# Kernel optimization log

Measured on AMD Instinct MI355X. Metric: run time of the kernel, lower is better.

## Reference

```python
import jax, jax.numpy as jnp
import numpy as np

B, L = 1024, 50
H = 512
N_ITEM, N_ENTITY, N_WORD = 50000, 100000, 30000


def setup_inputs() -> dict:
    key = jax.random.key(0)
    ks = jax.random.split(key, 16)
    inp = {
        "item_ids": jax.random.randint(ks[0], (B, L), 0, N_ITEM),
        "item_len": jax.random.randint(ks[1], (B,), 0, 51),
        "entity_ids": jax.random.randint(ks[2], (B, L), 0, N_ENTITY),
        "entity_len": jax.random.randint(ks[3], (B,), 0, 51),
        "word_ids": jax.random.randint(ks[4], (B, L), 0, N_WORD),
        "word_len": jax.random.randint(ks[5], (B,), 0, 51),
        "labels": jax.random.randint(ks[6], (B,), 0, N_ITEM),
        # learned parameters (torch default-ish init scales)
        "item_emb": jax.random.normal(ks[7], (N_ITEM, H), jnp.float32),
        "entity_emb": jax.random.normal(ks[8], (N_ENTITY, H), jnp.float32),
        "word_emb": jax.random.normal(ks[9], (N_WORD, H), jnp.float32),
        "W1": jax.random.normal(ks[10], (H, 4 * H), jnp.float32) / np.sqrt(H),
        "b1": jnp.zeros((4 * H,), jnp.float32),
        "W2": jax.random.normal(ks[11], (4 * H, N_ITEM), jnp.float32) / np.sqrt(4 * H),
        "b2": jnp.zeros((N_ITEM,), jnp.float32),
    }
    return inp


def _masked_mean(table, ids, lens):
    # segment-mean over ragged lists encoded as padded ids + lengths.
    # empty list -> zeros (matches the torch zero-fallback branch).
    mask = (jnp.arange(L)[None, :] < lens[:, None]).astype(table.dtype)  # [B,L]
    emb = table[ids]                                                     # [B,L,H]
    s = jnp.einsum("blh,bl->bh", emb, mask)
    denom = jnp.maximum(lens, 1).astype(table.dtype)[:, None]
    return s / denom


def reference(item_emb, entity_emb, word_emb, W1, b1, W2, b2,
              item_ids, item_len, entity_ids, entity_len,
              word_ids, word_len, labels):
    u = (_masked_mean(item_emb, item_ids, item_len)
         + _masked_mean(entity_emb, entity_ids, entity_len)
         + _masked_mean(word_emb, word_ids, word_len)) / 3.0   # [B,H]
    h = jax.nn.relu(u @ W1 + b1)                                # [B,4H]
    probs = jax.nn.softmax(h @ W2 + b2, axis=-1)                # [B,n_item]
    # faithful to source: CrossEntropyLoss applied on top of softmax outputs
    logp = jax.nn.log_softmax(probs, axis=-1)
    loss = -jnp.mean(jnp.take_along_axis(logp, labels[:, None], axis=-1))
    return probs, labels, loss
```

## Files before the change

kernel.cpp:

```cpp
#include <hip/hip_runtime.h>
#include <cstdint>
#include <cstddef>

typedef __attribute__((ext_vector_type(8))) short bf16x8;
typedef __attribute__((ext_vector_type(4))) float f32x4;

#define B_DIM 1024
#define L_SEQ 50
#define H_DIM 512
#define NITEM 50000
#define PSTRIDE 400

__device__ __forceinline__ unsigned short f2bf(float x) {
  unsigned u = __float_as_uint(x);
  return (unsigned short)((u + 0x7fffu + ((u >> 16) & 1u)) >> 16);
}
__device__ __forceinline__ unsigned pack2(float lo, float hi) {
  return (unsigned)f2bf(lo) | ((unsigned)f2bf(hi) << 16);
}
__device__ __forceinline__ void gld16(const unsigned short* g, unsigned short* l) {
  __builtin_amdgcn_global_load_lds((const __attribute__((address_space(1))) void*)g,
                                   (__attribute__((address_space(3))) void*)l, 16, 0, 0);
}
#define BAR() asm volatile("s_barrier" ::: "memory")

__device__ __forceinline__ void mean_body(int b2, const int* __restrict__ item_ids,
                                          const int* __restrict__ item_len,
                                          const int* __restrict__ ent_ids,
                                          const int* __restrict__ ent_len,
                                          const int* __restrict__ word_ids,
                                          const int* __restrict__ word_len,
                                          const float* __restrict__ item_emb,
                                          const float* __restrict__ ent_emb,
                                          const float* __restrict__ word_emb,
                                          unsigned short* __restrict__ u_bf) {
  const int b = b2 >> 1;
  const int col = ((b2 & 1) << 8) + threadIdx.x;
  float out = 0.f;
  {
    const int len = item_len[b]; float a = 0.f;
#pragma unroll 4
    for (int l = 0; l < len; ++l) a += item_emb[(size_t)item_ids[b * L_SEQ + l] * H_DIM + col];
    out += a / (float)(len > 0 ? len : 1);
  }
  {
    const int len = ent_len[b]; float a = 0.f;
#pragma unroll 4
    for (int l = 0; l < len; ++l) a += ent_emb[(size_t)ent_ids[b * L_SEQ + l] * H_DIM + col];
    out += a / (float)(len > 0 ? len : 1);
  }
  {
    const int len = word_len[b]; float a = 0.f;
#pragma unroll 4
    for (int l = 0; l < len; ++l) a += word_emb[(size_t)word_ids[b * L_SEQ + l] * H_DIM + col];
    out += a / (float)(len > 0 ? len : 1);
  }
  u_bf[b * H_DIM + col] = f2bf(out / 3.f);
}

__global__ void mean_kernel(const int* __restrict__ item_ids, const int* __restrict__ item_len,
                            const int* __restrict__ ent_ids, const int* __restrict__ ent_len,
                            const int* __restrict__ word_ids, const int* __restrict__ word_len,
                            const float* __restrict__ item_emb, const float* __restrict__ ent_emb,
                            const float* __restrict__ word_emb, unsigned short* __restrict__ u_bf) {
  mean_body(blockIdx.x, item_ids, item_len, ent_ids, ent_len, word_ids, word_len, item_emb,
            ent_emb, word_emb, u_bf);
}

__device__ __forceinline__ void transpose_body(const float* __restrict__ W,
                                               unsigned short* __restrict__ Wt, int K, int N,
                                               int k0, int n0, float (*tile)[65]) {
  const int tn = threadIdx.x & 63, tk = threadIdx.x >> 6;
  const int nv = (n0 + tn < N) ? n0 + tn : N - 1;
#pragma unroll
  for (int i = 0; i < 16; ++i)
    tile[tk + 4 * i][tn] = W[(size_t)(k0 + tk + 4 * i) * N + nv];
  __syncthreads();
  const int rn = threadIdx.x >> 2, ck = (threadIdx.x & 3) * 16;
  if (n0 + rn < N) {
    uint4 o[2];
    unsigned* po = (unsigned*)&o[0];
#pragma unroll
    for (int c = 0; c < 8; ++c)
      po[c] = pack2(tile[ck + 2 * c][rn], tile[ck + 2 * c + 1][rn]);
    *(uint4*)&Wt[(size_t)(n0 + rn) * K + k0 + ck] = o[0];
    *(uint4*)&Wt[(size_t)(n0 + rn) * K + k0 + ck + 8] = o[1];
  }
}

__global__ void prep_kernel(const int* __restrict__ item_ids, const int* __restrict__ item_len,
                            const int* __restrict__ ent_ids, const int* __restrict__ ent_len,
                            const int* __restrict__ word_ids, const int* __restrict__ word_len,
                            const float* __restrict__ item_emb, const float* __restrict__ ent_emb,
                            const float* __restrict__ word_emb, unsigned short* __restrict__ u_bf,
                            const float* __restrict__ W1, unsigned short* __restrict__ W1t,
                            const float* __restrict__ W2, unsigned short* __restrict__ W2t) {
  __shared__ float tile[64][65];
  const int b = blockIdx.x;
  if (b < 2048) {
    mean_body(b, item_ids, item_len, ent_ids, ent_len, word_ids, word_len, item_emb, ent_emb,
              word_emb, u_bf);
  } else if (b < 2048 + 25024) {
    const int t = b - 2048;
    transpose_body(W2, W2t, 2048, NITEM, (t & 31) * 64, (t >> 5) * 64, tile);
  } else {
    const int t = b - (2048 + 25024);
    transpose_body(W1, W1t, 512, 2048, (t & 7) * 64, (t >> 3) * 64, tile);
  }
}

template <int K, int N, int EPI>
__global__ __launch_bounds__(512, 1) void gemm256k(const unsigned short* __restrict__ Ag,
                                                   const unsigned short* __restrict__ Btg,
                                                   const float* __restrict__ bias,
                                                   unsigned short* __restrict__ Cbf,
                                                   float* __restrict__ Cf,
                                                   float* __restrict__ pmax,
                                                   float* __restrict__ psum) {
  __shared__ unsigned short lds[8 * 8192];
  unsigned short* Aring = lds;
  unsigned short* Bring = lds + 4 * 8192;

  const int tid = threadIdx.x;
  const int lane = tid & 63;
  const int wid = tid >> 6;

  const int nwg = gridDim.x;
  const int wgid = (blockIdx.x & 7) * (nwg >> 3) + (blockIdx.x >> 3);
  const int m0 = (wgid & 3) * 256;
  const int panel = wgid >> 2;
  const int n0 = panel * 256;

  const int r0 = (wid * 2) * 16 + (lane >> 2);
  const int r1 = r0 + 16;
  const int cg = (lane & 3) ^ ((lane >> 3) & 3);
  const unsigned short* pa0 = Ag + (size_t)(m0 + r0) * K + cg * 8;
  const unsigned short* pa1 = Ag + (size_t)(m0 + r1) * K + cg * 8;
  int rg0 = n0 + r0; rg0 = rg0 < N ? rg0 : N - 1;
  int rg1 = n0 + r1; rg1 = rg1 < N ? rg1 : N - 1;
  const unsigned short* pb0 = Btg + (size_t)rg0 * K + cg * 8;
  const unsigned short* pb1 = Btg + (size_t)rg1 * K + cg * 8;
  const int li0 = wid * 2, li1 = wid * 2 + 1;

  const int wr = wid >> 2, wc = wid & 3;
  const int l15 = lane & 15, kb = lane >> 4;
  f32x4 acc[8][4] = {};

  const int HS = K / 32;
#pragma unroll
  for (int hh = 0; hh < 3; ++hh) {
    const int ko = hh * 32, sl = hh & 3;
    gld16(pa0 + ko, &Aring[sl * 8192 + li0 * 512]);
    gld16(pa1 + ko, &Aring[sl * 8192 + li1 * 512]);
    gld16(pb0 + ko, &Bring[sl * 8192 + li0 * 512]);
    gld16(pb1 + ko, &Bring[sl * 8192 + li1 * 512]);
  }
  asm volatile("s_waitcnt vmcnt(8)" ::: "memory");
  BAR();

#pragma unroll 1
  for (int h = 0; h < HS; ++h) {
    const int slot = h & 3;
    const int nslot = (h + 3) & 3;
    const int kst = (h + 3) * 32;
    const bool st = (h + 3) < HS;
    const unsigned short* As_ = &Aring[slot * 8192];
    const unsigned short* Bs_ = &Bring[slot * 8192];

    bf16x8 afA[4], bfr[4];
#pragma unroll
    for (int i = 0; i < 4; ++i) {
      const int row = wr * 128 + i * 16 + l15;
      afA[i] = *(const bf16x8*)&As_[row * 32 + (kb ^ ((row >> 1) & 3)) * 8];
    }
#pragma unroll
    for (int j = 0; j < 4; ++j) {
      const int col = wc * 64 + j * 16 + l15;
      bfr[j] = *(const bf16x8*)&Bs_[col * 32 + (kb ^ ((col >> 1) & 3)) * 8];
    }
    if (st) {
      gld16(pa0 + kst, &Aring[nslot * 8192 + li0 * 512]);
      gld16(pa1 + kst, &Aring[nslot * 8192 + li1 * 512]);
    }
    BAR();
    __builtin_amdgcn_s_setprio(1);
#pragma unroll
    for (int i = 0; i < 4; ++i)
#pragma unroll
      for (int j = 0; j < 4; ++j)
        acc[i][j] = __builtin_amdgcn_mfma_f32_16x16x32_bf16(afA[i], bfr[j], acc[i][j], 0, 0, 0);
    __builtin_amdgcn_s_setprio(0);
    BAR();

    bf16x8 afB[4];
#pragma unroll
    for (int i = 0; i < 4; ++i) {
      const int row = wr * 128 + (i + 4) * 16 + l15;
      afB[i] = *(const bf16x8*)&As_[row * 32 + (kb ^ ((row >> 1) & 3)) * 8];
    }
    if (st) {
      gld16(pb0 + kst, &Bring[nslot * 8192 + li0 * 512]);
      gld16(pb1 + kst, &Bring[nslot * 8192 + li1 * 512]);
    }
    BAR();
    __builtin_amdgcn_s_setprio(1);
#pragma unroll
    for (int i = 0; i < 4; ++i)
#pragma unroll
      for (int j = 0; j < 4; ++j)
        acc[i + 4][j] =
            __builtin_amdgcn_mfma_f32_16x16x32_bf16(afB[i], bfr[j], acc[i + 4][j], 0, 0, 0);
    __builtin_amdgcn_s_setprio(0);

    if (h + 1 < HS) {
      if (h + 4 <= HS)
        asm volatile("s_waitcnt vmcnt(8)" ::: "memory");
      else if (h + 3 == HS)
        asm volatile("s_waitcnt vmcnt(4)" ::: "memory");
      else
        asm volatile("s_waitcnt vmcnt(0)" ::: "memory");
      BAR();
    }
  }

  float bv[4];
  bool val[4];
#pragma unroll
  for (int j = 0; j < 4; ++j) {
    const int cgl = n0 + wc * 64 + 16 * j + l15;
    val[j] = (cgl < N);
    bv[j] = bias[val[j] ? cgl : 0];
  }
#pragma unroll
  for (int i = 0; i < 8; ++i) {
    const int rbase = m0 + wr * 128 + 16 * i + 4 * kb;
#pragma unroll
    for (int j = 0; j < 4; ++j) {
      if (val[j]) {
        const int cgl = n0 + wc * 64 + 16 * j + l15;
#pragma unroll
        for (int rr = 0; rr < 4; ++rr) {
          const float v = acc[i][j][rr] + bv[j];
          if (EPI == 0)
            Cbf[(size_t)(rbase + rr) * N + cgl] = f2bf(v > 0.f ? v : 0.f);
          else
            Cf[(size_t)(rbase + rr) * N + cgl] = v;
        }
      }
    }
  }

  if constexpr (EPI == 1) {
    __syncthreads();
    float* redm = (float*)&lds[0];
    float* reds = redm + 1024;
#pragma unroll
    for (int i = 0; i < 8; ++i) {
#pragma unroll
      for (int rr = 0; rr < 4; ++rr) {
        float mx = -3.0e38f;
#pragma unroll
        for (int j = 0; j < 4; ++j)
          if (val[j]) mx = fmaxf(mx, acc[i][j][rr] + bv[j]);
#pragma unroll
        for (int d = 1; d < 16; d <<= 1) mx = fmaxf(mx, __shfl_xor(mx, d));
        float s = 0.f;
#pragma unroll
        for (int j = 0; j < 4; ++j)
          if (val[j]) s += expf(acc[i][j][rr] + bv[j] - mx);
#pragma unroll
        for (int d = 1; d < 16; d <<= 1) s += __shfl_xor(s, d);
        if (l15 == 0) {
          const int rw = wr * 128 + 16 * i + 4 * kb + rr;
          redm[wc * 256 + rw] = mx;
          reds[wc * 256 + rw] = s;
        }
      }
    }
    __syncthreads();
    if (tid < 256) {
      float mm = redm[tid], ss = reds[tid];
#pragma unroll
      for (int w = 1; w < 4; ++w) {
        const float ma = redm[w * 256 + tid], sa = reds[w * 256 + tid];
        const float nm = fmaxf(mm, ma);
        ss = ss * expf(mm - nm) + sa * expf(ma - nm);
        mm = nm;
      }
      pmax[(size_t)(m0 + tid) * PSTRIDE + panel] = mm;
      psum[(size_t)(m0 + tid) * PSTRIDE + panel] = ss;
    }
  }
}

template <int K, int N, int EPI, int PBASE>
__global__ __launch_bounds__(512, 1) void gemm128x256(const unsigned short* __restrict__ Ag,
                                                      const unsigned short* __restrict__ Btg,
                                                      const float* __restrict__ bias,
                                                      unsigned short* __restrict__ Cbf,
                                                      float* __restrict__ Cf,
                                                      float* __restrict__ pmax,
                                                      float* __restrict__ psum) {
  __shared__ unsigned short lds[4 * 4096 + 4 * 8192];
  unsigned short* Aring = lds;
  unsigned short* Bring = lds + 4 * 4096;

  const int tid = threadIdx.x;
  const int lane = tid & 63;
  const int wid = tid >> 6;

  const int nwg = gridDim.x;
  const int wgid = (blockIdx.x & 7) * (nwg >> 3) + (blockIdx.x >> 3);
  const int m0 = (wgid & 7) * 128;
  const int panel = wgid >> 3;
  const int n0 = (PBASE + panel) * 256;

  const int cg = (lane & 3) ^ ((lane >> 3) & 3);
  const int arow = wid * 16 + (lane >> 2);
  const unsigned short* pa = Ag + (size_t)(m0 + arow) * K + cg * 8;
  const int br0 = wid * 32 + (lane >> 2), br1 = br0 + 16;
  int rg0 = n0 + br0; rg0 = rg0 < N ? rg0 : N - 1;
  int rg1 = n0 + br1; rg1 = rg1 < N ? rg1 : N - 1;
  const unsigned short* pb0 = Btg + (size_t)rg0 * K + cg * 8;
  const unsigned short* pb1 = Btg + (size_t)rg1 * K + cg * 8;
  const int li0 = wid * 2, li1 = wid * 2 + 1;

  const int wr = wid >> 2, wc = wid & 3;
  const int l15 = lane & 15, kb = lane >> 4;
  f32x4 acc[4][4] = {};

  const int HS = K / 32;
#pragma unroll
  for (int hh = 0; hh < 3; ++hh) {
    const int ko = hh * 32;
    gld16(pa + ko, &Aring[hh * 4096 + wid * 512]);
    gld16(pb0 + ko, &Bring[hh * 8192 + li0 * 512]);
    gld16(pb1 + ko, &Bring[hh * 8192 + li1 * 512]);
  }
  asm volatile("s_waitcnt vmcnt(6)" ::: "memory");
  BAR();

#pragma unroll 1
  for (int h = 0; h < HS; ++h) {
    const int slot = h & 3;
    const int nslot = (h + 3) & 3;
    const int kst = (h + 3) * 32;
    const unsigned short* As_ = &Aring[slot * 4096];
    const unsigned short* Bs_ = &Bring[slot * 8192];

    if (h + 3 < HS) {
      gld16(pa + kst, &Aring[nslot * 4096 + wid * 512]);
      gld16(pb0 + kst, &Bring[nslot * 8192 + li0 * 512]);
      gld16(pb1 + kst, &Bring[nslot * 8192 + li1 * 512]);
    }

    bf16x8 af[4], bf[4];
#pragma unroll
    for (int i = 0; i < 4; ++i) {
      const int row = wr * 64 + i * 16 + l15;
      af[i] = *(const bf16x8*)&As_[row * 32 + (kb ^ ((row >> 1) & 3)) * 8];
    }
#pragma unroll
    for (int j = 0; j < 4; ++j) {
      const int col = wc * 64 + j * 16 + l15;
      bf[j] = *(const bf16x8*)&Bs_[col * 32 + (kb ^ ((col >> 1) & 3)) * 8];
    }
    __builtin_amdgcn_s_setprio(1);
#pragma unroll
    for (int i = 0; i < 4; ++i)
#pragma unroll
      for (int j = 0; j < 4; ++j)
        acc[i][j] = __builtin_amdgcn_mfma_f32_16x16x32_bf16(af[i], bf[j], acc[i][j], 0, 0, 0);
    __builtin_amdgcn_s_setprio(0);

    if (h + 1 < HS) {
      if (h + 4 <= HS)
        asm volatile("s_waitcnt vmcnt(6)" ::: "memory");
      else if (h + 3 == HS)
        asm volatile("s_waitcnt vmcnt(3)" ::: "memory");
      else
        asm volatile("s_waitcnt vmcnt(0)" ::: "memory");
      BAR();
    }
  }

  float bv[4];
  bool val[4];
#pragma unroll
  for (int j = 0; j < 4; ++j) {
    const int cgl = n0 + wc * 64 + 16 * j + l15;
    val[j] = (cgl < N);
    bv[j] = bias[val[j] ? cgl : 0];
  }
#pragma unroll
  for (int i = 0; i < 4; ++i) {
    const int rbase = m0 + wr * 64 + 16 * i + 4 * kb;
#pragma unroll
    for (int j = 0; j < 4; ++j) {
      if (val[j]) {
        const int cgl = n0 + wc * 64 + 16 * j + l15;
#pragma unroll
        for (int rr = 0; rr < 4; ++rr) {
          const float v = acc[i][j][rr] + bv[j];
          if (EPI == 0)
            Cbf[(size_t)(rbase + rr) * N + cgl] = f2bf(v > 0.f ? v : 0.f);
          else
            Cf[(size_t)(rbase + rr) * N + cgl] = v;
        }
      }
    }
  }

  if constexpr (EPI == 1) {
    __syncthreads();
    float* redm = (float*)&lds[0];
    float* reds = redm + 512;
#pragma unroll
    for (int i = 0; i < 4; ++i) {
#pragma unroll
      for (int rr = 0; rr < 4; ++rr) {
        float mx = -3.0e38f;
#pragma unroll
        for (int j = 0; j < 4; ++j)
          if (val[j]) mx = fmaxf(mx, acc[i][j][rr] + bv[j]);
#pragma unroll
        for (int d = 1; d < 16; d <<= 1) mx = fmaxf(mx, __shfl_xor(mx, d));
        float s = 0.f;
#pragma unroll
        for (int j = 0; j < 4; ++j)
          if (val[j]) s += expf(acc[i][j][rr] + bv[j] - mx);
#pragma unroll
        for (int d = 1; d < 16; d <<= 1) s += __shfl_xor(s, d);
        if (l15 == 0) {
          const int rw = wr * 64 + 16 * i + 4 * kb + rr;
          redm[wc * 128 + rw] = mx;
          reds[wc * 128 + rw] = s;
        }
      }
    }
    __syncthreads();
    if (tid < 128) {
      float mm = redm[tid], ss = reds[tid];
#pragma unroll
      for (int w = 1; w < 4; ++w) {
        const float ma = redm[w * 128 + tid], sa = reds[w * 128 + tid];
        const float nm = fmaxf(mm, ma);
        ss = ss * expf(mm - nm) + sa * expf(ma - nm);
        mm = nm;
      }
      pmax[(size_t)(m0 + tid) * PSTRIDE + PBASE + panel] = mm;
      psum[(size_t)(m0 + tid) * PSTRIDE + PBASE + panel] = ss;
    }
  }
}

template <int K, int N, int EPI>
__global__ __launch_bounds__(256, 2) void gemm128(const unsigned short* __restrict__ Ag,
                                                  const unsigned short* __restrict__ Btg,
                                                  const float* __restrict__ bias,
                                                  unsigned short* __restrict__ Cbf,
                                                  float* __restrict__ Cf) {
  __shared__ unsigned short As[2][128 * 64];
  __shared__ unsigned short Bs[2][128 * 64];
  const int tid = threadIdx.x;
  const int lane = tid & 63;
  const int wid = tid >> 6;
  const int nwg = gridDim.x;
  const int wgid = (blockIdx.x & 7) * (nwg >> 3) + (blockIdx.x >> 3);
  const int m0 = (wgid & 7) * 128;
  const int n0 = (wgid >> 3) * 128;
  const int srsub = lane >> 3;
  const int scg = (lane & 7) ^ srsub;
  const unsigned short* pa[4];
  const unsigned short* pb[4];
#pragma unroll
  for (int qq = 0; qq < 4; ++qq) {
    const int seg = wid * 4 + qq;
    const int row = seg * 8 + srsub;
    pa[qq] = Ag + (size_t)(m0 + row) * K + scg * 8;
    int rg = n0 + row;
    rg = rg < N ? rg : N - 1;
    pb[qq] = Btg + (size_t)rg * K + scg * 8;
  }
  auto stage = [&](int t, int s) {
    const int ko = t * 64;
#pragma unroll
    for (int qq = 0; qq < 4; ++qq) {
      const int seg = wid * 4 + qq;
      gld16(pa[qq] + ko, &As[s][seg * 512]);
      gld16(pb[qq] + ko, &Bs[s][seg * 512]);
    }
  };
  const int wr = wid >> 1, wc = wid & 1;
  const int l15 = lane & 15, kb = lane >> 4;
  f32x4 acc[4][4] = {};
  auto compute = [&](int s) {
#pragma unroll
    for (int koi = 0; koi < 2; ++koi) {
      bf16x8 af[4], bf[4];
#pragma unroll
      for (int i = 0; i < 4; ++i) {
        const int row = wr * 64 + i * 16 + l15;
        af[i] = *(const bf16x8*)&As[s][row * 64 + ((koi * 4 + kb) ^ (row & 7)) * 8];
      }
#pragma unroll
      for (int j = 0; j < 4; ++j) {
        const int col = wc * 64 + j * 16 + l15;
        bf[j] = *(const bf16x8*)&Bs[s][col * 64 + ((koi * 4 + kb) ^ (col & 7)) * 8];
      }
#pragma unroll
      for (int i = 0; i < 4; ++i)
#pragma unroll
        for (int j = 0; j < 4; ++j)
          acc[i][j] = __builtin_amdgcn_mfma_f32_16x16x32_bf16(af[i], bf[j], acc[i][j], 0, 0, 0);
    }
  };
  const int NT = K / 64;
  stage(0, 0);
  asm volatile("s_waitcnt vmcnt(0)" ::: "memory");
  __syncthreads();
#pragma unroll 1
  for (int t = 0; t < NT; ++t) {
    if (t + 1 < NT) stage(t + 1, (t + 1) & 1);
    compute(t & 1);
    asm volatile("s_waitcnt vmcnt(0)" ::: "memory");
    __syncthreads();
  }
  float bv[4];
  bool val[4];
#pragma unroll
  for (int j = 0; j < 4; ++j) {
    const int cg2 = n0 + wc * 64 + 16 * j + l15;
    val[j] = (cg2 < N);
    bv[j] = bias[val[j] ? cg2 : 0];
  }
#pragma unroll
  for (int i = 0; i < 4; ++i) {
    const int rbase = m0 + wr * 64 + 16 * i + 4 * kb;
#pragma unroll
    for (int j = 0; j < 4; ++j) {
      if (val[j]) {
        const int cg2 = n0 + wc * 64 + 16 * j + l15;
#pragma unroll
        for (int rr = 0; rr < 4; ++rr) {
          const float v = acc[i][j][rr] + bv[j];
          if (EPI == 0)
            Cbf[(size_t)(rbase + rr) * N + cg2] = f2bf(v > 0.f ? v : 0.f);
          else
            Cf[(size_t)(rbase + rr) * N + cg2] = v;
        }
      }
    }
  }
}

template <int K, int N, int EPI>
__global__ __launch_bounds__(512, 2) void gemm_fused(const unsigned short* __restrict__ Ag,
                                                     const float* __restrict__ Bg,
                                                     const float* __restrict__ bias,
                                                     unsigned short* __restrict__ Cbf,
                                                     float* __restrict__ Cf,
                                                     float* __restrict__ pmax,
                                                     float* __restrict__ psum) {
  __shared__ unsigned short As[2][256 * 64];
  __shared__ uint4 Bs[2][8 * 128];
  const int tid = threadIdx.x;
  const int lane = tid & 63;
  const int wid = tid >> 6;
  const int m0 = blockIdx.x * 256;
  const int n0 = blockIdx.y * 128;
  const int arow = tid >> 3;
  const int ach = tid & 7;
  const int bn = 2 * lane;
  const int bk = 8 * wid;
  const int bcolg = (n0 + bn < N - 2) ? (n0 + bn) : (N - 2);
  uint4 areg[4];
  float2 breg[8];
  f32x4 acc[4][4] = {};
  auto stage_global = [&](int kt) {
    const int k0 = kt * 64;
#pragma unroll
    for (int qq = 0; qq < 4; ++qq)
      areg[qq] = *(const uint4*)&Ag[(size_t)(m0 + arow + 64 * qq) * K + k0 + 8 * ach];
#pragma unroll
    for (int i = 0; i < 8; ++i) breg[i] = *(const float2*)&Bg[(size_t)(k0 + bk + i) * N + bcolg];
  };
  auto stage_lds = [&](int buf) {
#pragma unroll
    for (int qq = 0; qq < 4; ++qq) {
      const int row = arow + 64 * qq;
      *(uint4*)&As[buf][row * 64 + ((8 * ach) ^ ((row & 7) * 8))] = areg[qq];
    }
    uint4 c0, c1;
    c0.x = pack2(breg[0].x, breg[1].x); c0.y = pack2(breg[2].x, breg[3].x);
    c0.z = pack2(breg[4].x, breg[5].x); c0.w = pack2(breg[6].x, breg[7].x);
    c1.x = pack2(breg[0].y, breg[1].y); c1.y = pack2(breg[2].y, breg[3].y);
    c1.z = pack2(breg[4].y, breg[5].y); c1.w = pack2(breg[6].y, breg[7].y);
    Bs[buf][wid * 128 + bn] = c0;
    Bs[buf][wid * 128 + bn + 1] = c1;
  };
  const int wr = wid & 3, wc = wid >> 2;
  const int mw = 64 * wr, nw = 64 * wc;
  const int l15 = lane & 15, kb = lane >> 4;
  auto compute = [&](int buf) {
#pragma unroll
    for (int koi = 0; koi < 2; ++koi) {
      bf16x8 af[4], bfv[4];
#pragma unroll
      for (int i = 0; i < 4; ++i) {
        const int row = mw + 16 * i + l15;
        af[i] = *(const bf16x8*)&As[buf][row * 64 + ((32 * koi + 8 * kb) ^ ((row & 7) * 8))];
      }
#pragma unroll
      for (int j = 0; j < 4; ++j)
        bfv[j] = *(const bf16x8*)&Bs[buf][(4 * koi + kb) * 128 + nw + 16 * j + l15];
#pragma unroll
      for (int i = 0; i < 4; ++i)
#pragma unroll
        for (int j = 0; j < 4; ++j)
          acc[i][j] = __builtin_amdgcn_mfma_f32_16x16x32_bf16(af[i], bfv[j], acc[i][j], 0, 0, 0);
    }
  };
  const int NT = K / 64;
  stage_global(0);
  stage_lds(0);
  __syncthreads();
  for (int t = 0; t < NT; ++t) {
    const int cur = t & 1;
    if (t + 1 < NT) stage_global(t + 1);
    compute(cur);
    if (t + 1 < NT) stage_lds(cur ^ 1);
    __syncthreads();
  }
  float bv[4];
  bool val[4];
#pragma unroll
  for (int j = 0; j < 4; ++j) {
    const int cg2 = n0 + nw + 16 * j + l15;
    val[j] = (cg2 < N);
    bv[j] = bias[val[j] ? cg2 : 0];
  }
#pragma unroll
  for (int i = 0; i < 4; ++i) {
    const int rbase = m0 + mw + 16 * i + 4 * kb;
#pragma unroll
    for (int j = 0; j < 4; ++j) {
      if (val[j]) {
        const int cg2 = n0 + nw + 16 * j + l15;
#pragma unroll
        for (int rr = 0; rr < 4; ++rr) {
          const float v = acc[i][j][rr] + bv[j];
          if (EPI == 0)
            Cbf[(size_t)(rbase + rr) * N + cg2] = f2bf(v > 0.f ? v : 0.f);
          else
            Cf[(size_t)(rbase + rr) * N + cg2] = v;
        }
      }
    }
  }
  if constexpr (EPI == 1) {
    float* redm = (float*)&As[0][0];
    float* reds = redm + 512;
#pragma unroll
    for (int i = 0; i < 4; ++i) {
#pragma unroll
      for (int rr = 0; rr < 4; ++rr) {
        float mx = -3.0e38f;
#pragma unroll
        for (int j = 0; j < 4; ++j)
          if (val[j]) mx = fmaxf(mx, acc[i][j][rr] + bv[j]);
#pragma unroll
        for (int d = 1; d < 16; d <<= 1) mx = fmaxf(mx, __shfl_xor(mx, d));
        float s = 0.f;
#pragma unroll
        for (int j = 0; j < 4; ++j)
          if (val[j]) s += expf(acc[i][j][rr] + bv[j] - mx);
#pragma unroll
        for (int d = 1; d < 16; d <<= 1) s += __shfl_xor(s, d);
        if (l15 == 0) {
          const int rl = mw + 16 * i + 4 * kb + rr;
          redm[wc * 256 + rl] = mx;
          reds[wc * 256 + rl] = s;
        }
      }
    }
    __syncthreads();
    if (tid < 256) {
      const float ma = redm[tid], mb = redm[256 + tid];
      const float mm = fmaxf(ma, mb);
      const float ss = reds[tid] * expf(ma - mm) + reds[256 + tid] * expf(mb - mm);
      pmax[(size_t)(m0 + tid) * PSTRIDE + blockIdx.y] = mm;
      psum[(size_t)(m0 + tid) * PSTRIDE + blockIdx.y] = ss;
    }
  }
}

__global__ void smax1r(const float* __restrict__ pmax, const float* __restrict__ psum,
                       float* __restrict__ rms, int ntiles) {
  const int b = blockIdx.x;
  const int l = threadIdx.x;
  float m = -3.4e38f, s = 0.f;
  for (int i = l; i < ntiles; i += 64) {
    const float pm = pmax[(size_t)b * PSTRIDE + i];
    const float ps = psum[(size_t)b * PSTRIDE + i];
    const float nm = fmaxf(m, pm);
    s = s * expf(m - nm) + ps * expf(pm - nm);
    m = nm;
  }
  for (int d = 1; d < 64; d <<= 1) {
    const float om = __shfl_xor(m, d), os = __shfl_xor(s, d);
    const float nm = fmaxf(m, om);
    s = s * expf(m - nm) + os * expf(om - nm);
    m = nm;
  }
  if (l == 0) {
    rms[b] = m;
    rms[B_DIM + b] = s;
  }
}

__global__ void smax2(float* __restrict__ buf, const float* __restrict__ rms,
                      const int* __restrict__ labels, float* __restrict__ row_lp) {
  const int b = blockIdx.x;
  float4* p = (float4*)(buf + (size_t)b * NITEM);
  const float m = rms[b];
  const float inv = 1.f / rms[B_DIM + b];
  const int lab = labels[b];
  __shared__ float s_pl;
  __shared__ float ss[256];
  float s2 = 0.f;
  for (int i = threadIdx.x; i < NITEM / 4; i += 256) {
    const float4 v = p[i];
    float pr[4];
#pragma unroll
    for (int j = 0; j < 4; ++j) {
      pr[j] = expf((&v.x)[j] - m) * inv;
      s2 += expf(pr[j] - inv);
    }
    float4 w;
    w.x = pr[0]; w.y = pr[1]; w.z = pr[2]; w.w = pr[3];
    p[i] = w;
    if ((lab >> 2) == i) s_pl = pr[lab & 3];
  }
  ss[threadIdx.x] = s2;
  __syncthreads();
  for (int off = 128; off > 0; off >>= 1) {
    if (threadIdx.x < off) ss[threadIdx.x] += ss[threadIdx.x + off];
    __syncthreads();
  }
  if (threadIdx.x == 0) row_lp[b] = s_pl - (inv + logf(ss[0]));
}

__global__ void fin(const float* __restrict__ row_lp, const int* __restrict__ labels,
                    float* __restrict__ out) {
  __shared__ float sb[256];
  float a = 0.f;
  for (int i = threadIdx.x; i < B_DIM; i += 256) {
    a += row_lp[i];
    out[(size_t)B_DIM * NITEM + i] = (float)labels[i];
  }
  sb[threadIdx.x] = a;
  __syncthreads();
  for (int off = 128; off > 0; off >>= 1) {
    if (threadIdx.x < off) sb[threadIdx.x] += sb[threadIdx.x + off];
    __syncthreads();
  }
  if (threadIdx.x == 0) out[(size_t)B_DIM * NITEM + B_DIM] = -sb[0] / (float)B_DIM;
}

extern "C" void kernel_launch(void* const* d_in, const int* in_sizes, int n_in,
                              void* d_out, int out_size, void* d_ws, size_t ws_size,
                              hipStream_t stream) {
  const int* item_ids = (const int*)d_in[0];
  const int* item_len = (const int*)d_in[1];
  const int* ent_ids = (const int*)d_in[2];
  const int* ent_len = (const int*)d_in[3];
  const int* word_ids = (const int*)d_in[4];
  const int* word_len = (const int*)d_in[5];
  const int* labels = (const int*)d_in[6];
  const float* item_emb = (const float*)d_in[7];
  const float* ent_emb = (const float*)d_in[8];
  const float* word_emb = (const float*)d_in[9];
  const float* W1 = (const float*)d_in[10];
  const float* b1 = (const float*)d_in[11];
  const float* W2 = (const float*)d_in[12];
  const float* b2 = (const float*)d_in[13];

  float* out = (float*)d_out;
  char* ws = (char*)d_ws;
  unsigned short* u_bf = (unsigned short*)ws;
  unsigned short* h_bf = (unsigned short*)(ws + (1 << 20));
  float* pmax = (float*)(ws + 5 * (1 << 20));
  float* psum = (float*)(ws + 7 * (1 << 20));
  float* rms = (float*)(ws + 9 * (1 << 20));
  float* row_lp = rms + 2 * B_DIM;
  unsigned short* W1t = (unsigned short*)(ws + 10 * (1 << 20));
  unsigned short* W2t = (unsigned short*)(ws + 16 * (1 << 20));
  float* logits = out;

  const size_t need = (size_t)16 * (1 << 20) + (size_t)NITEM * 2048 * 2;
  const bool fast = ws_size >= need;

  if (fast) {
    prep_kernel<<<2048 + 25024 + 256, 256, 0, stream>>>(item_ids, item_len, ent_ids, ent_len,
                                                        word_ids, word_len, item_emb, ent_emb,
                                                        word_emb, u_bf, W1, W1t, W2, W2t);
    gemm128<512, 2048, 0><<<8 * 16, 256, 0, stream>>>(u_bf, W1t, b1, h_bf, nullptr);
    gemm256k<2048, NITEM, 1><<<768, 512, 0, stream>>>(h_bf, W2t, b2, nullptr, logits, pmax,
                                                      psum);
    gemm128x256<2048, NITEM, 1, 192><<<32, 512, 0, stream>>>(h_bf, W2t, b2, nullptr, logits,
                                                             pmax, psum);
    smax1r<<<B_DIM, 64, 0, stream>>>(pmax, psum, rms, 196);
  } else {
    mean_kernel<<<2 * B_DIM, 256, 0, stream>>>(item_ids, item_len, ent_ids, ent_len, word_ids,
                                               word_len, item_emb, ent_emb, word_emb, u_bf);
    gemm_fused<512, 2048, 0><<<dim3(4, 16), 512, 0, stream>>>(u_bf, W1, b1, h_bf, nullptr,
                                                              nullptr, nullptr);
    gemm_fused<2048, NITEM, 1><<<dim3(4, 391), 512, 0, stream>>>(h_bf, W2, b2, nullptr, logits,
                                                                 pmax, psum);
    smax1r<<<B_DIM, 64, 0, stream>>>(pmax, psum, rms, 391);
  }
  smax2<<<B_DIM, 256, 0, stream>>>(logits, rms, labels, row_lp);
  fin<<<1, 256, 0, stream>>>(row_lp, labels, out);
}
```

Baseline: 562.3 us.

## Load B operand directly from global into registers, staging only A in LDS

The big W2 GEMM now streams B fragments from global memory straight into registers, double-buffered across even and odd k-steps, and stages only the A tile in an LDS ring. This halves LDS usage and drops the mid-step barriers and B LDS reads, leaving one barrier per k-step. The cost is that every wave of the four in a column re-reads the same B columns from global or L2 without LDS sharing, and the B loads are uncoalesced 16-byte per-lane accesses with the latency held in registers.

```diff
diff --git a/kernel.cpp b/kernel.cpp
--- a/kernel.cpp
+++ b/kernel.cpp
@@ -110,16 +110,14 @@
 }
 
 template <int K, int N, int EPI>
-__global__ __launch_bounds__(512, 1) void gemm256k(const unsigned short* __restrict__ Ag,
+__global__ __launch_bounds__(512, 1) void gemm256r(const unsigned short* __restrict__ Ag,
                                                    const unsigned short* __restrict__ Btg,
                                                    const float* __restrict__ bias,
                                                    unsigned short* __restrict__ Cbf,
                                                    float* __restrict__ Cf,
                                                    float* __restrict__ pmax,
                                                    float* __restrict__ psum) {
-  __shared__ unsigned short lds[8 * 8192];
-  unsigned short* Aring = lds;
-  unsigned short* Bring = lds + 4 * 8192;
+  __shared__ unsigned short Aring[4 * 8192];
 
   const int tid = threadIdx.x;
   const int lane = tid & 63;
@@ -131,97 +129,87 @@
   const int panel = wgid >> 2;
   const int n0 = panel * 256;
 
-  const int r0 = (wid * 2) * 16 + (lane >> 2);
+  const int r0 = wid * 32 + (lane >> 2);
   const int r1 = r0 + 16;
   const int cg = (lane & 3) ^ ((lane >> 3) & 3);
   const unsigned short* pa0 = Ag + (size_t)(m0 + r0) * K + cg * 8;
   const unsigned short* pa1 = Ag + (size_t)(m0 + r1) * K + cg * 8;
-  int rg0 = n0 + r0; rg0 = rg0 < N ? rg0 : N - 1;
-  int rg1 = n0 + r1; rg1 = rg1 < N ? rg1 : N - 1;
-  const unsigned short* pb0 = Btg + (size_t)rg0 * K + cg * 8;
-  const unsigned short* pb1 = Btg + (size_t)rg1 * K + cg * 8;
   const int li0 = wid * 2, li1 = wid * 2 + 1;
 
   const int wr = wid >> 2, wc = wid & 3;
   const int l15 = lane & 15, kb = lane >> 4;
+
+  const unsigned short* pbf[4];
+#pragma unroll
+  for (int j = 0; j < 4; ++j) {
+    int r = n0 + wc * 64 + 16 * j + l15;
+    r = r < N ? r : N - 1;
+    pbf[j] = Btg + (size_t)r * K + kb * 8;
+  }
+
   f32x4 acc[8][4] = {};
+  uint4 bE[4], bO[4];
 
   const int HS = K / 32;
 #pragma unroll
-  for (int hh = 0; hh < 3; ++hh) {
-    const int ko = hh * 32, sl = hh & 3;
-    gld16(pa0 + ko, &Aring[sl * 8192 + li0 * 512]);
-    gld16(pa1 + ko, &Aring[sl * 8192 + li1 * 512]);
-    gld16(pb0 + ko, &Bring[sl * 8192 + li0 * 512]);
-    gld16(pb1 + ko, &Bring[sl * 8192 + li1 * 512]);
-  }
-  asm volatile("s_waitcnt vmcnt(8)" ::: "memory");
+  for (int j = 0; j < 4; ++j) bE[j] = *(const uint4*)&pbf[j][0];
+#pragma unroll
+  for (int j = 0; j < 4; ++j) bO[j] = *(const uint4*)&pbf[j][32];
+  gld16(pa0, &Aring[li0 * 512]);
+  gld16(pa1, &Aring[li1 * 512]);
+  gld16(pa0 + 32, &Aring[8192 + li0 * 512]);
+  gld16(pa1 + 32, &Aring[8192 + li1 * 512]);
+  gld16(pa0 + 64, &Aring[2 * 8192 + li0 * 512]);
+  gld16(pa1 + 64, &Aring[2 * 8192 + li1 * 512]);
+  asm volatile("s_waitcnt vmcnt(0)" ::: "memory");
   BAR();
 
+#define GSTEP(h, bcur)                                                                   \
+  {                                                                                      \
+    const unsigned short* As_ = &Aring[((h) & 3) * 8192];                                \
+    bf16x8 af[8];                                                                        \
+    _Pragma("unroll") for (int i = 0; i < 8; ++i) {                                      \
+      const int row = wr * 128 + i * 16 + l15;                                           \
+      af[i] = *(const bf16x8*)&As_[row * 32 + (kb ^ ((row >> 1) & 3)) * 8];              \
+    }                                                                                    \
+    __builtin_amdgcn_s_setprio(1);                                                       \
+    _Pragma("unroll") for (int i = 0; i < 8; ++i) {                                      \
+      acc[i][0] = __builtin_amdgcn_mfma_f32_16x16x32_bf16(af[i], *(bf16x8*)&bcur[0],     \
+                                                          acc[i][0], 0, 0, 0);           \
+      acc[i][1] = __builtin_amdgcn_mfma_f32_16x16x32_bf16(af[i], *(bf16x8*)&bcur[1],     \
+                                                          acc[i][1], 0, 0, 0);           \
+      acc[i][2] = __builtin_amdgcn_mfma_f32_16x16x32_bf16(af[i], *(bf16x8*)&bcur[2],     \
+                                                          acc[i][2], 0, 0, 0);           \
+      acc[i][3] = __builtin_amdgcn_mfma_f32_16x16x32_bf16(af[i], *(bf16x8*)&bcur[3],     \
+                                                          acc[i][3], 0, 0, 0);           \
+    }                                                                                    \
+    __builtin_amdgcn_s_setprio(0);                                                       \
+    if ((h) + 2 < HS) {                                                                  \
+      _Pragma("unroll") for (int j = 0; j < 4; ++j) bcur[j] =                            \
+          *(const uint4*)&pbf[j][((h) + 2) * 32];                                        \
+    }                                                                                    \
+    if ((h) + 3 < HS) {                                                                  \
+      unsigned short* d = &Aring[(((h) + 3) & 3) * 8192];                                \
+      gld16(pa0 + ((h) + 3) * 32, d + li0 * 512);                                        \
+      gld16(pa1 + ((h) + 3) * 32, d + li1 * 512);                                        \
+    }                                                                                    \
+    if ((h) + 1 < HS) {                                                                  \
+      if ((h) + 4 <= HS)                                                                 \
+        asm volatile("s_waitcnt vmcnt(6)" ::: "memory");                                 \
+      else if ((h) + 3 == HS)                                                            \
+        asm volatile("s_waitcnt vmcnt(4)" ::: "memory");                                 \
+      else                                                                               \
+        asm volatile("s_waitcnt vmcnt(0)" ::: "memory");                                 \
+      BAR();                                                                             \
+    }                                                                                    \
+  }
+
 #pragma unroll 1
-  for (int h = 0; h < HS; ++h) {
-    const int slot = h & 3;
-    const int nslot = (h + 3) & 3;
-    const int kst = (h + 3) * 32;
-    const bool st = (h + 3) < HS;
-    const unsigned short* As_ = &Aring[slot * 8192];
-    const unsigned short* Bs_ = &Bring[slot * 8192];
-
-    bf16x8 afA[4], bfr[4];
-#pragma unroll
-    for (int i = 0; i < 4; ++i) {
-      const int row = wr * 128 + i * 16 + l15;
-      afA[i] = *(const bf16x8*)&As_[row * 32 + (kb ^ ((row >> 1) & 3)) * 8];
-    }
-#pragma unroll
-    for (int j = 0; j < 4; ++j) {
-      const int col = wc * 64 + j * 16 + l15;
-      bfr[j] = *(const bf16x8*)&Bs_[col * 32 + (kb ^ ((col >> 1) & 3)) * 8];
-    }
-    if (st) {
-      gld16(pa0 + kst, &Aring[nslot * 8192 + li0 * 512]);
-      gld16(pa1 + kst, &Aring[nslot * 8192 + li1 * 512]);
-    }
-    BAR();
-    __builtin_amdgcn_s_setprio(1);
-#pragma unroll
-    for (int i = 0; i < 4; ++i)
-#pragma unroll
-      for (int j = 0; j < 4; ++j)
-        acc[i][j] = __builtin_amdgcn_mfma_f32_16x16x32_bf16(afA[i], bfr[j], acc[i][j], 0, 0, 0);
-    __builtin_amdgcn_s_setprio(0);
-    BAR();
-
-    bf16x8 afB[4];
-#pragma unroll
-    for (int i = 0; i < 4; ++i) {
-      const int row = wr * 128 + (i + 4) * 16 + l15;
-      afB[i] = *(const bf16x8*)&As_[row * 32 + (kb ^ ((row >> 1) & 3)) * 8];
-    }
-    if (st) {
-      gld16(pb0 + kst, &Bring[nslot * 8192 + li0 * 512]);
-      gld16(pb1 + kst, &Bring[nslot * 8192 + li1 * 512]);
-    }
-    BAR();
-    __builtin_amdgcn_s_setprio(1);
-#pragma unroll
-    for (int i = 0; i < 4; ++i)
-#pragma unroll
-      for (int j = 0; j < 4; ++j)
-        acc[i + 4][j] =
-            __builtin_amdgcn_mfma_f32_16x16x32_bf16(afB[i], bfr[j], acc[i + 4][j], 0, 0, 0);
-    __builtin_amdgcn_s_setprio(0);
-
-    if (h + 1 < HS) {
-      if (h + 4 <= HS)
-        asm volatile("s_waitcnt vmcnt(8)" ::: "memory");
-      else if (h + 3 == HS)
-        asm volatile("s_waitcnt vmcnt(4)" ::: "memory");
-      else
-        asm volatile("s_waitcnt vmcnt(0)" ::: "memory");
-      BAR();
-    }
-  }
+  for (int hh = 0; hh < HS; hh += 2) {
+    GSTEP(hh, bE);
+    GSTEP(hh + 1, bO);
+  }
+#undef GSTEP
 
   float bv[4];
   bool val[4];
@@ -252,7 +240,7 @@
 
   if constexpr (EPI == 1) {
     __syncthreads();
-    float* redm = (float*)&lds[0];
+    float* redm = (float*)&Aring[0];
     float* reds = redm + 1024;
 #pragma unroll
     for (int i = 0; i < 8; ++i) {
@@ -806,7 +794,7 @@
                                                         word_ids, word_len, item_emb, ent_emb,
                                                         word_emb, u_bf, W1, W1t, W2, W2t);
     gemm128<512, 2048, 0><<<8 * 16, 256, 0, stream>>>(u_bf, W1t, b1, h_bf, nullptr);
-    gemm256k<2048, NITEM, 1><<<768, 512, 0, stream>>>(h_bf, W2t, b2, nullptr, logits, pmax,
+    gemm256r<2048, NITEM, 1><<<768, 512, 0, stream>>>(h_bf, W2t, b2, nullptr, logits, pmax,
                                                       psum);
     gemm128x256<2048, NITEM, 1, 192><<<32, 512, 0, stream>>>(h_bf, W2t, b2, nullptr, logits,
                                                              pmax, psum);
```

Result: slower. 627.0 us (+11.5%).
